# Kernel optimization log

Measured on AMD Instinct MI355X. Metric: run time of the kernel, lower is better.

The kernel has to match this reference:

```python
import jax, jax.numpy as jnp
import numpy as np

DIM = 128
B, NQ, NK = 4, 4096, 4096
SCALE = DIM ** -0.5


def setup_inputs() -> dict:
    key = jax.random.key(0)
    ks = jax.random.split(key, 13)
    def lin(k, shape, scale=0.02):
        return jax.random.normal(k, shape, dtype=jnp.float32) * scale
    return {
        "query": jax.random.normal(ks[0], (B, NQ, DIM), dtype=jnp.float32),
        "key": jax.random.normal(ks[1], (B, NK, DIM), dtype=jnp.float32),
        "value": jax.random.normal(ks[2], (B, NK, DIM), dtype=jnp.float32),
        "att_bias": jax.random.normal(ks[3], (B, NK), dtype=jnp.float32),
        # params, [in, out] layout (torch Linear is x @ W.T + b)
        "q_w": lin(ks[4], (DIM, DIM)), "q_b": jnp.zeros((DIM,), jnp.float32),
        "k_w": lin(ks[5], (DIM, DIM)),
        "v_w": lin(ks[6], (DIM, DIM)), "v_b": jnp.zeros((DIM,), jnp.float32),
        "vs_w": lin(ks[7], (DIM, 1)), "vs_b": jnp.zeros((1,), jnp.float32),
        "p_w": lin(ks[8], (DIM, DIM)), "p_b": jnp.zeros((DIM,), jnp.float32),
    }


def reference(query, key, value, att_bias, q_w, q_b, k_w, v_w, v_b, vs_w, vs_b, p_w, p_b):
    # projections
    q = query @ q_w + q_b                      # [B, NQ, D]
    k = key @ k_w                              # [B, NK, D] (no bias)
    v = value @ v_w + v_b                      # [B, NK, D]
    # per-key semantic scalar, broadcast over queries: [B, 1, NK]
    semantic = (value @ vs_w + vs_b).reshape(value.shape[0], 1, value.shape[1])
    # scores + biases
    attn = jnp.einsum('bqd,bkd->bqk', q, k) * SCALE + semantic
    attn = attn + att_bias[:, None, :]
    attn = jax.nn.softmax(attn, axis=-1)
    out = jnp.einsum('bqk,bkd->bqd', attn, v)  # [B, NQ, D]
    out = out @ p_w + p_b
    return out
```

## Files before the change

kernel.cpp:

```cpp
#include <hip/hip_runtime.h>

typedef __bf16 bf16x8 __attribute__((ext_vector_type(8)));
typedef float f32x4 __attribute__((ext_vector_type(4)));
typedef float f32x16 __attribute__((ext_vector_type(16)));

#define MFMA16(a,b,c) __builtin_amdgcn_mfma_f32_16x16x32_bf16(a,b,c,0,0,0)
#define MFMA32(a,b,c) __builtin_amdgcn_mfma_f32_32x32x16_bf16(a,b,c,0,0,0)

static __device__ __forceinline__ unsigned short f2bf(float f){
  union{float f;unsigned u;}v; v.f=f;
  unsigned u=v.u;
  u += 0x7fffu + ((u>>16)&1u);
  return (unsigned short)(u>>16);
}
static __device__ __forceinline__ float bf2f(unsigned short h){
  union{unsigned u;float f;}v; v.u=((unsigned)h)<<16; return v.f;
}
static __device__ __forceinline__ unsigned cvtpk(float lo, float hi){
  unsigned r;
  asm("v_cvt_pk_bf16_f32 %0, %1, %2" : "=v"(r) : "v"(lo), "v"(hi));
  return r;
}
static __device__ __forceinline__ void gload16(const void* g, void* l){
  __builtin_amdgcn_global_load_lds(
    (const __attribute__((address_space(1))) unsigned int*)(uintptr_t)g,
    (__attribute__((address_space(3))) unsigned int*)(uintptr_t)l,
    16, 0, 0);
}

#define SCALE_QK 0.08838834764831845f
#define LOG2E    1.44269504088896340f
#define M0_L2    16.0f

#define SWZ128(r,c) (((r)<<7) + ((c) ^ (((r)&7)<<3)))


__global__ __launch_bounds__(256) void k_proj(
    const float* __restrict__ query, const float* __restrict__ key,
    const float* __restrict__ value, const float* __restrict__ att_bias,
    const float* __restrict__ q_w, const float* __restrict__ q_b,
    const float* __restrict__ k_w, const float* __restrict__ v_w,
    const float* __restrict__ v_b, const float* __restrict__ vs_w,
    const float* __restrict__ vs_b,
    unsigned short* __restrict__ qp, unsigned short* __restrict__ kp,
    unsigned short* __restrict__ vpt, float* __restrict__ biasc)
{
  const int t = blockIdx.y;
  const float* X = (t==0) ? query : ((t==1) ? key : value);
  const float* W = (t==0) ? q_w  : ((t==1) ? k_w : v_w);
  const int tid = threadIdx.x;
  const int row0 = blockIdx.x * 64;

  __shared__ __align__(16) unsigned short Wt[128][136];
  __shared__ __align__(16) unsigned short Xs[64][136];
  __shared__ float vsw_s[128];

  #pragma unroll 4
  for (int i=0;i<16;i++){
    int idx = tid*64 + i*4;
    float4 v4 = *(const float4*)(W + idx);
    Wt[(idx+0)&127][(idx+0)>>7] = f2bf(v4.x);
    Wt[(idx+1)&127][(idx+1)>>7] = f2bf(v4.y);
    Wt[(idx+2)&127][(idx+2)>>7] = f2bf(v4.z);
    Wt[(idx+3)&127][(idx+3)>>7] = f2bf(v4.w);
  }
  {
    const float* Xb = X + (size_t)row0*128;
    #pragma unroll
    for (int i=0;i<8;i++){
      int f4 = i*256 + tid;
      int row = f4>>5, c4 = f4&31;
      float4 v = *(const float4*)(Xb + row*128 + c4*4);
      ushort4 h;
      h.x = f2bf(v.x); h.y = f2bf(v.y); h.z = f2bf(v.z); h.w = f2bf(v.w);
      *(ushort4*)&Xs[row][c4*4] = h;
    }
  }
  if (t==2 && tid<128) vsw_s[tid] = vs_w[tid];
  __syncthreads();

  const int w = tid>>6, lane = tid&63, lr = lane&15, lg = lane>>4;
  f32x4 acc[8];
  #pragma unroll
  for (int nt=0;nt<8;nt++) acc[nt] = (f32x4){0.f,0.f,0.f,0.f};
  #pragma unroll
  for (int kk=0;kk<4;kk++){
    bf16x8 a = *(const bf16x8*)&Xs[w*16+lr][kk*32+lg*8];
    #pragma unroll
    for (int nt=0;nt<8;nt++){
      bf16x8 bb = *(const bf16x8*)&Wt[nt*16+lr][kk*32+lg*8];
      acc[nt] = MFMA16(a,bb,acc[nt]);
    }
  }

  if (t < 2){
    const float* bias = (t==0) ? q_b : (const float*)nullptr;
    const float sc = (t==0) ? (SCALE_QK*LOG2E) : 1.f;
    unsigned short* dstm = (t==0) ? qp : kp;
    #pragma unroll
    for (int nt=0;nt<8;nt++){
      int col = nt*16+lr;
      float bv = bias ? bias[col] : 0.f;
      #pragma unroll
      for (int r=0;r<4;r++){
        int row = row0 + w*16 + lg*4 + r;
        dstm[(size_t)row*128+col] = f2bf((acc[nt][r] + bv) * sc);
      }
    }
  } else {
    {
      int rl = tid>>2, part = tid&3;
      float s = 0.f;
      #pragma unroll
      for (int j=0;j<32;j++){
        int d = part*32+j;
        s += bf2f(Xs[rl][d]) * vsw_s[d];
      }
      s += __shfl_xor(s,1);
      s += __shfl_xor(s,2);
      if ((tid&3)==0){
        int rg = row0 + rl;
        biasc[rg] = (s + vs_b[0] + att_bias[rg]) * LOG2E - M0_L2;
      }
    }
    __syncthreads();
    unsigned short* Vls = (unsigned short*)Wt;
    #pragma unroll
    for (int nt=0;nt<8;nt++){
      int col = nt*16+lr;
      float bv = v_b[col];
      #pragma unroll
      for (int r=0;r<4;r++){
        int rl_ = w*16 + lg*4 + r;
        int k5 = rl_ & 31;
        int pos = 16*(k5>>4) + (k5&3) + 4*((k5>>3)&1) + 8*((k5>>2)&1);
        int np = (rl_ & 32) | pos;
        Vls[col*72 + np] = f2bf(acc[nt][r] + bv);
      }
    }
    __syncthreads();
    int d = tid>>1, half = tid&1;
    int bi = row0>>12, n0 = row0&4095;
    unsigned short* dst = vpt + ((size_t)(bi*128+d))*4096 + n0 + half*32;
    const unsigned short* src = Vls + d*72 + half*32;
    #pragma unroll
    for (int i=0;i<4;i++)
      *(uint4*)(dst + i*8) = *(const uint4*)(src + i*8);
  }
}

__global__ __launch_bounds__(256,3) void k_flash(
    const unsigned short* __restrict__ qp, const unsigned short* __restrict__ kp,
    const unsigned short* __restrict__ vpt, const float* __restrict__ biasc,
    unsigned short* __restrict__ opart, float* __restrict__ ml)
{
  const int f = blockIdx.x;
  const int xcd = f & 7, slot = f >> 3;
  const int group = xcd*4 + (slot>>5);
  const int b = group>>3, split = group&7;
  const int q0 = (slot & 31) * 128;

  const int tid = threadIdx.x;
  const int w = tid>>6, lane = tid&63;
  const int l31 = lane&31, hi = lane>>5;

  __shared__ __align__(16) unsigned short Ks[2][32*128];
  __shared__ __align__(16) char Vp[2][8192];
  __shared__ __align__(16) float Bs[512];

  const unsigned short* kbase = kp  + (size_t)(b*4096 + split*512)*128;
  const char* vbase = (const char*)(vpt + (size_t)b*128*4096 + split*512);
  const float* bbase = biasc + b*4096 + split*512;

  if (w < 2) gload16(bbase + w*256 + lane*4, (char*)Bs + w*1024);

  bf16x8 qf[8];
  {
    const unsigned short* qrow = qp + ((size_t)(b*4096 + q0 + w*32 + l31))*128;
    #pragma unroll
    for (int kk=0;kk<8;kk++) qf[kk] = *(const bf16x8*)(qrow + kk*16 + hi*8);
  }

  #define STAGE(bf_, k0_) do{                                                 \
    const char* kb_ = (const char*)kbase + (size_t)(k0_)*256;                 \
    const char* vb_ = vbase + (size_t)(k0_)*2;                                \
    _Pragma("unroll")                                                         \
    for (int i=0;i<2;i++){                                                    \
      int s_ = w*2+i;                                                         \
      int kr = s_*4 + (lane>>4);                                              \
      gload16(kb_ + kr*256 + (((lane&15)*16) ^ ((kr&7)*16)),                  \
              (char*)Ks[bf_] + s_*1024);                                      \
      int u_ = (lane&7) ^ ((lane>>3)&7);                                      \
      int vd = s_*16 + ((lane>>3)<<1) + (u_>>2);                              \
      gload16(vb_ + (size_t)vd*8192 + ((u_&3)<<4),                            \
              (char*)Vp[bf_] + s_*1024);                                      \
    }                                                                         \
  }while(0)

  float l_run = 0.f;
  f32x16 acc[4];
  #pragma unroll
  for (int dt=0;dt<4;dt++) acc[dt] = (f32x16){};

  STAGE(0, 0);
  __syncthreads();

  const int vA = (l31>>1)*128;
  const int vX = ((l31>>1)&7)<<4;
  const int vH = (l31&1)*64 + hi*16;

  for (int t=0;t<16;t++){
    const int cur = t & 1;
    if (t<15) STAGE(cur^1, (t+1)*32);

    const unsigned short* Kc = Ks[cur];
    const char* Vc = Vp[cur];

    const float* Bt = &Bs[t*32];
    float4 b0 = *(const float4*)&Bt[hi*4];
    float4 b1 = *(const float4*)&Bt[8 + hi*4];
    float4 b2 = *(const float4*)&Bt[16 + hi*4];
    float4 b3 = *(const float4*)&Bt[24 + hi*4];
    f32x16 sc;
    sc[0]=b0.x;  sc[1]=b0.y;  sc[2]=b0.z;  sc[3]=b0.w;
    sc[4]=b1.x;  sc[5]=b1.y;  sc[6]=b1.z;  sc[7]=b1.w;
    sc[8]=b2.x;  sc[9]=b2.y;  sc[10]=b2.z; sc[11]=b2.w;
    sc[12]=b3.x; sc[13]=b3.y; sc[14]=b3.z; sc[15]=b3.w;

    __builtin_amdgcn_s_setprio(1);
    #pragma unroll
    for (int kk=0;kk<8;kk++){
      bf16x8 a = *(const bf16x8*)&Kc[SWZ128(l31, kk*16 + hi*8)];
      sc = MFMA32(a, qf[kk], sc);
    }
    __builtin_amdgcn_s_setprio(0);

    float rs = 0.f;
    #pragma unroll
    for (int i=0;i<16;i++){
      sc[i] = __builtin_exp2f(sc[i]); rs += sc[i];
    }
    rs += __shfl_xor(rs, 32);
    l_run += rs;

    {
      union { unsigned u[4]; bf16x8 v; } pu0;
      pu0.u[0] = cvtpk(sc[0], sc[1]);
      pu0.u[1] = cvtpk(sc[2], sc[3]);
      pu0.u[2] = cvtpk(sc[4], sc[5]);
      pu0.u[3] = cvtpk(sc[6], sc[7]);
      __builtin_amdgcn_s_setprio(1);
      #pragma unroll
      for (int dt=0;dt<4;dt++){
        bf16x8 v0 = *(const bf16x8*)(Vc + dt*2048 + vA + ((vH +  0) ^ vX));
        acc[dt] = MFMA32(pu0.v, v0, acc[dt]);
      }
      __builtin_amdgcn_s_setprio(0);
    }
    {
      union { unsigned u[4]; bf16x8 v; } pu1;
      pu1.u[0] = cvtpk(sc[8],  sc[9]);
      pu1.u[1] = cvtpk(sc[10], sc[11]);
      pu1.u[2] = cvtpk(sc[12], sc[13]);
      pu1.u[3] = cvtpk(sc[14], sc[15]);
      __builtin_amdgcn_s_setprio(1);
      #pragma unroll
      for (int dt=0;dt<4;dt++){
        bf16x8 v1 = *(const bf16x8*)(Vc + dt*2048 + vA + ((vH + 32) ^ vX));
        acc[dt] = MFMA32(pu1.v, v1, acc[dt]);
      }
      __builtin_amdgcn_s_setprio(0);
    }

    __syncthreads();
  }
  #undef STAGE

  const size_t rowbase = (size_t)split*16384 + (size_t)b*4096 + q0;
  #pragma unroll
  for (int r=0;r<16;r++){
    int qn = (r&3) + 8*(r>>2) + 4*hi;
    float inv = 1.f/__shfl(l_run, qn);
    size_t row = rowbase + w*32 + qn;
    opart[row*128 +      l31] = f2bf(acc[0][r]*inv);
    opart[row*128 + 32 + l31] = f2bf(acc[1][r]*inv);
    opart[row*128 + 64 + l31] = f2bf(acc[2][r]*inv);
    opart[row*128 + 96 + l31] = f2bf(acc[3][r]*inv);
  }
  if (hi==0){
    size_t rg = rowbase + w*32 + l31;
    ml[rg*2]   = 0.f;
    ml[rg*2+1] = l_run;
  }
}

__global__ __launch_bounds__(256) void k_outproj(
    const unsigned short* __restrict__ opart, const float* __restrict__ ml,
    const float* __restrict__ p_w, const float* __restrict__ p_b,
    float* __restrict__ out)
{
  const int tid = threadIdx.x;
  const int row0 = blockIdx.x*32;
  __shared__ __align__(16) unsigned short Wt[128][136];
  __shared__ __align__(16) unsigned short Xs[32][136];
  __shared__ float wmg[8][32];

  #pragma unroll 4
  for (int i=0;i<16;i++){
    int idx = tid*64 + i*4;
    float4 v4 = *(const float4*)(p_w + idx);
    Wt[(idx+0)&127][(idx+0)>>7] = f2bf(v4.x);
    Wt[(idx+1)&127][(idx+1)>>7] = f2bf(v4.y);
    Wt[(idx+2)&127][(idx+2)>>7] = f2bf(v4.z);
    Wt[(idx+3)&127][(idx+3)>>7] = f2bf(v4.w);
  }
  if (tid < 32){
    int row = row0 + tid;
    float m[8], l[8];
    #pragma unroll
    for (int i=0;i<8;i++){
      m[i] = ml[((size_t)i*16384 + row)*2];
      l[i] = ml[((size_t)i*16384 + row)*2 + 1];
    }
    float M = m[0];
    #pragma unroll
    for (int i=1;i<8;i++) M = fmaxf(M, m[i]);
    float wi[8], wsum = 0.f;
    #pragma unroll
    for (int i=0;i<8;i++){ wi[i] = __builtin_exp2f(m[i]-M)*l[i]; wsum += wi[i]; }
    float inv = 1.f/wsum;
    #pragma unroll
    for (int i=0;i<8;i++) wmg[i][tid] = wi[i]*inv;
  }
  __syncthreads();
  #pragma unroll
  for (int i=0;i<2;i++){
    int e = (i*256 + tid)*8;
    int row = e>>7, col = e&127;
    float a8[8];
    #pragma unroll
    for (int j=0;j<8;j++) a8[j] = 0.f;
    #pragma unroll
    for (int s=0;s<8;s++){
      uint4 v = *(const uint4*)(opart + ((size_t)s*16384 + row0 + row)*128 + col);
      float wv = wmg[s][row];
      const unsigned short* hp = (const unsigned short*)&v;
      #pragma unroll
      for (int j=0;j<8;j++) a8[j] += wv * bf2f(hp[j]);
    }
    unsigned short h8[8];
    #pragma unroll
    for (int j=0;j<8;j++) h8[j] = f2bf(a8[j]);
    *(uint4*)&Xs[row][col] = *(const uint4*)h8;
  }
  __syncthreads();

  const int w=tid>>6, lane=tid&63, lr=lane&15, lg=lane>>4;
  const int r0 = (w&1)*16, c0 = (w>>1)*64;
  f32x4 acc[4];
  #pragma unroll
  for (int nt=0;nt<4;nt++) acc[nt] = (f32x4){0.f,0.f,0.f,0.f};
  #pragma unroll
  for (int kk=0;kk<4;kk++){
    bf16x8 a = *(const bf16x8*)&Xs[r0+lr][kk*32+lg*8];
    #pragma unroll
    for (int nt=0;nt<4;nt++){
      bf16x8 bb = *(const bf16x8*)&Wt[c0+nt*16+lr][kk*32+lg*8];
      acc[nt] = MFMA16(a,bb,acc[nt]);
    }
  }
  __syncthreads();
  float* Os = (float*)Wt;
  #pragma unroll
  for (int nt=0;nt<4;nt++){
    int col = c0 + nt*16 + lr;
    float pb = p_b[col];
    #pragma unroll
    for (int r=0;r<4;r++){
      int row = r0 + lg*4 + r;
      Os[row*132 + col] = acc[nt][r] + pb;
    }
  }
  __syncthreads();
  {
    int row = tid>>3, seg = tid&7;
    const float* src = Os + row*132 + seg*16;
    float* dst = out + (size_t)(row0+row)*128 + seg*16;
    #pragma unroll
    for (int i=0;i<4;i++)
      *(float4*)(dst + i*4) = *(const float4*)(src + i*4);
  }
}

extern "C" void kernel_launch(void* const* d_in, const int* in_sizes, int n_in,
                              void* d_out, int out_size, void* d_ws, size_t ws_size,
                              hipStream_t stream) {
  (void)in_sizes; (void)n_in; (void)out_size; (void)ws_size;
  const float* query    = (const float*)d_in[0];
  const float* key      = (const float*)d_in[1];
  const float* value    = (const float*)d_in[2];
  const float* att_bias = (const float*)d_in[3];
  const float* q_w = (const float*)d_in[4];
  const float* q_b = (const float*)d_in[5];
  const float* k_w = (const float*)d_in[6];
  const float* v_w = (const float*)d_in[7];
  const float* v_b = (const float*)d_in[8];
  const float* vs_w = (const float*)d_in[9];
  const float* vs_b = (const float*)d_in[10];
  const float* p_w = (const float*)d_in[11];
  const float* p_b = (const float*)d_in[12];

  char* ws = (char*)d_ws;
  unsigned short* qp    = (unsigned short*)(ws);
  unsigned short* kp    = (unsigned short*)(ws + 4194304);
  unsigned short* vpt   = (unsigned short*)(ws + 8388608);
  float*          biasc = (float*)(ws + 12582912);
  unsigned short* opart = (unsigned short*)(ws + 12648448);
  float*          ml    = (float*)(ws + 46202880);

  hipLaunchKernelGGL(k_proj, dim3(256,3), dim3(256), 0, stream,
    query,key,value,att_bias,q_w,q_b,k_w,v_w,v_b,vs_w,vs_b,qp,kp,vpt,biasc);
  hipLaunchKernelGGL(k_flash, dim3(1024), dim3(256), 0, stream,
    qp,kp,vpt,biasc,opart,ml);
  hipLaunchKernelGGL(k_outproj, dim3(512), dim3(256), 0, stream,
    opart,ml,p_w,p_b,(float*)d_out);
}
```

Before: 78.82 us.

## Split keys six ways with uneven tile counts to fill one wave of workgroups

Result: faster. 75.00 us (-4.8%).

```diff
diff --git a/kernel.cpp b/kernel.cpp
--- a/kernel.cpp
+++ b/kernel.cpp
@@ -31,6 +31,8 @@
 #define SCALE_QK 0.08838834764831845f
 #define LOG2E    1.44269504088896340f
 #define M0_L2    16.0f
+
+#define NSPLIT   6
 
 #define SWZ128(r,c) (((r)<<7) + ((c) ^ (((r)&7)<<3)))
 
@@ -156,9 +158,11 @@
 {
   const int f = blockIdx.x;
   const int xcd = f & 7, slot = f >> 3;
-  const int group = xcd*4 + (slot>>5);
-  const int b = group>>3, split = group&7;
+  const int group = xcd*3 + (slot>>5);
+  const int b = group/NSPLIT, split = group%NSPLIT;
   const int q0 = (slot & 31) * 128;
+  const int ts = 21*split + (split<2 ? split : 2);
+  const int nt = (split<2) ? 22 : 21;
 
   const int tid = threadIdx.x;
   const int w = tid>>6, lane = tid&63;
@@ -166,13 +170,13 @@
 
   __shared__ __align__(16) unsigned short Ks[2][32*128];
   __shared__ __align__(16) char Vp[2][8192];
-  __shared__ __align__(16) float Bs[512];
-
-  const unsigned short* kbase = kp  + (size_t)(b*4096 + split*512)*128;
-  const char* vbase = (const char*)(vpt + (size_t)b*128*4096 + split*512);
-  const float* bbase = biasc + b*4096 + split*512;
-
-  if (w < 2) gload16(bbase + w*256 + lane*4, (char*)Bs + w*1024);
+  __shared__ __align__(16) float Bs[768];
+
+  const unsigned short* kbase = kp  + (size_t)(b*4096 + ts*32)*128;
+  const char* vbase = (const char*)(vpt + (size_t)b*128*4096 + ts*32);
+  const float* bbase = biasc + b*4096 + ts*32;
+
+  if (w < 3) gload16(bbase + w*256 + lane*4, (char*)Bs + w*1024);
 
   bf16x8 qf[8];
   {
@@ -209,9 +213,9 @@
   const int vX = ((l31>>1)&7)<<4;
   const int vH = (l31&1)*64 + hi*16;
 
-  for (int t=0;t<16;t++){
+  for (int t=0;t<nt;t++){
     const int cur = t & 1;
-    if (t<15) STAGE(cur^1, (t+1)*32);
+    if (t<nt-1) STAGE(cur^1, (t+1)*32);
 
     const unsigned short* Kc = Ks[cur];
     const char* Vc = Vp[cur];
@@ -303,7 +307,7 @@
   const int row0 = blockIdx.x*32;
   __shared__ __align__(16) unsigned short Wt[128][136];
   __shared__ __align__(16) unsigned short Xs[32][136];
-  __shared__ float wmg[8][32];
+  __shared__ float wmg[NSPLIT][32];
 
   #pragma unroll 4
   for (int i=0;i<16;i++){
@@ -316,21 +320,15 @@
   }
   if (tid < 32){
     int row = row0 + tid;
-    float m[8], l[8];
-    #pragma unroll
-    for (int i=0;i<8;i++){
-      m[i] = ml[((size_t)i*16384 + row)*2];
+    float l[NSPLIT], wsum = 0.f;
+    #pragma unroll
+    for (int i=0;i<NSPLIT;i++){
       l[i] = ml[((size_t)i*16384 + row)*2 + 1];
-    }
-    float M = m[0];
-    #pragma unroll
-    for (int i=1;i<8;i++) M = fmaxf(M, m[i]);
-    float wi[8], wsum = 0.f;
-    #pragma unroll
-    for (int i=0;i<8;i++){ wi[i] = __builtin_exp2f(m[i]-M)*l[i]; wsum += wi[i]; }
+      wsum += l[i];
+    }
     float inv = 1.f/wsum;
     #pragma unroll
-    for (int i=0;i<8;i++) wmg[i][tid] = wi[i]*inv;
+    for (int i=0;i<NSPLIT;i++) wmg[i][tid] = l[i]*inv;
   }
   __syncthreads();
   #pragma unroll
@@ -341,7 +339,7 @@
     #pragma unroll
     for (int j=0;j<8;j++) a8[j] = 0.f;
     #pragma unroll
-    for (int s=0;s<8;s++){
+    for (int s=0;s<NSPLIT;s++){
       uint4 v = *(const uint4*)(opart + ((size_t)s*16384 + row0 + row)*128 + col);
       float wv = wmg[s][row];
       const unsigned short* hp = (const unsigned short*)&v;
@@ -420,7 +418,7 @@
 
   hipLaunchKernelGGL(k_proj, dim3(256,3), dim3(256), 0, stream,
     query,key,value,att_bias,q_w,q_b,k_w,v_w,v_b,vs_w,vs_b,qp,kp,vpt,biasc);
-  hipLaunchKernelGGL(k_flash, dim3(1024), dim3(256), 0, stream,
+  hipLaunchKernelGGL(k_flash, dim3(768), dim3(256), 0, stream,
     qp,kp,vpt,biasc,opart,ml);
   hipLaunchKernelGGL(k_outproj, dim3(512), dim3(256), 0, stream,
     opart,ml,p_w,p_b,(float*)d_out);
```
